# Kernel optimization log

Measured on AMD Instinct MI355X. Metric: run time of the kernel, lower is better.

## Reference

```python
import jax, jax.numpy as jnp
import numpy as np

B, P, V, M = 4, 4, 4096, 2048
BIG = 1e10  # masking constant for invalid points in min-reductions


def setup_inputs() -> dict:
    key = jax.random.key(0)
    k1, k2, k3, k4, k5 = jax.random.split(key, 5)
    vertices = jax.random.normal(k1, (B, V, 3), jnp.float32)
    # 3x4 projection matrices; force the 3rd row so w = 0.05*z + 4 > 0 (no divide blowup)
    projmats = 0.5 * jax.random.normal(k2, (P, 3, 4), jnp.float32)
    projmats = projmats.at[:, 2, :].set(jnp.array([0.0, 0.0, 0.05, 4.0], jnp.float32))
    edgemaps = jax.random.normal(k3, (B, P, M, 2), jnp.float32)
    boundary_mask = jax.random.bernoulli(k4, 0.3, (B, P, V))
    edgemaps_len = jax.random.randint(k5, (B, P), M // 2, M + 1, jnp.int32)
    return {"vertices": vertices, "projmats": projmats, "edgemaps": edgemaps,
            "boundary_mask": boundary_mask, "edgemaps_len": edgemaps_len}


def reference(vertices, projmats, edgemaps, boundary_mask, edgemaps_len):
    # --- project vertices into all views (homogeneous + perspective divide) ---
    ones = jnp.ones(vertices.shape[:2] + (1,), vertices.dtype)
    vh = jnp.concatenate([vertices, ones], axis=-1)              # (B,V,4)
    proj = jnp.einsum('pij,bvj->bpvi', projmats, vh)             # (B,P,V,3)
    pts = proj[..., :2] / proj[..., 2:3]                         # (B,P,V,2)

    # --- masked pairwise squared distances (GEMM-form, no (.,.,2) broadcast) ---
    x2 = jnp.sum(pts * pts, axis=-1)                             # (B,P,V)
    y2 = jnp.sum(edgemaps * edgemaps, axis=-1)                   # (B,P,M)
    xy = jnp.einsum('bpvc,bpmc->bpvm', pts, edgemaps)            # (B,P,V,M)
    d2 = jnp.maximum(x2[..., :, None] + y2[..., None, :] - 2.0 * xy, 0.0)

    xmask = boundary_mask.astype(d2.dtype)                       # (B,P,V)
    ymask = (jnp.arange(M)[None, None, :] < edgemaps_len[..., None]).astype(d2.dtype)

    # min over valid targets / valid boundary points
    cham_x = jnp.min(jnp.where(ymask[:, :, None, :] > 0, d2, BIG), axis=-1)  # (B,P,V)
    cham_y = jnp.min(jnp.where(xmask[:, :, :, None] > 0, d2, BIG), axis=-2)  # (B,P,M)

    x_len = jnp.maximum(jnp.sum(xmask, axis=-1), 1.0)            # (B,P)
    y_len = jnp.maximum(jnp.sum(ymask, axis=-1), 1.0)            # (B,P)
    loss_p = jnp.sum(xmask * cham_x, -1) / x_len + jnp.sum(ymask * cham_y, -1) / y_len
    return jnp.mean(loss_p, axis=-1)                             # (B,) per-mesh chamfer loss
```

## Files before the change

kernel.cpp:

```cpp
#include <hip/hip_runtime.h>
#include <stdint.h>

namespace {
constexpr int B = 4, P = 4, V = 4096, M = 2048;
constexpr int BP = B * P;
constexpr float BIGF = 1e10f;
constexpr int TPB   = 256;
constexpr int OTILE = 128;
constexpr int XT = V / OTILE;
constexpr int YT = M / OTILE;
constexpr int ROLES = XT + YT;
constexpr int NBLK = BP * ROLES;
constexpr int UN = 8;
constexpr int KPB = 4;
constexpr int VPB = V / KPB;
constexpr int MPB = M / KPB;
}


__global__ __launch_bounds__(256) void prep_kernel(
    const float* __restrict__ vertices,
    const float* __restrict__ projmats,
    const uint8_t* __restrict__ maskraw,
    const float* __restrict__ edgemaps,
    int* __restrict__ nvalid,
    float* __restrict__ sx,
    float* __restrict__ sy,
    int* __restrict__ done,
    float4* __restrict__ pnk,
    float4* __restrict__ epk)
{
    const int bp = blockIdx.x / KPB;
    const int k  = blockIdx.x % KPB;
    const int b = bp / P, p = bp % P;
    const int tid = threadIdx.x;
    const int lane = tid & 63;
    const int wave = tid >> 6;

    __shared__ int s_res[4];
    __shared__ int s_cnt;
    __shared__ int s_prew[4];
    if (tid < 4) { s_res[tid] = 0; s_prew[tid] = 0; }
    if (tid == 0) s_cnt = 0;
    __syncthreads();

    uint32_t loc[4] = {0u, 0u, 0u, 0u};
    const int NB = 16384;
    for (int i = tid * 16; i < NB; i += 256 * 16) {
        const uint32_t* w = (const uint32_t*)(maskraw + i);
        const uint32_t orw = w[0] | w[1] | w[2] | w[3];
        loc[0] |= orw & 0x000000FFu;
        loc[1] |= orw & 0x0000FF00u;
        loc[2] |= orw & 0x00FF0000u;
        loc[3] |= orw & 0xFF000000u;
    }
    #pragma unroll
    for (int j = 0; j < 4; ++j)
        if (loc[j]) atomicOr(&s_res[j], 1);
    __syncthreads();
    int layout;
    if (!s_res[1] && !s_res[2] && !s_res[3]) layout = 1;
    else if (!s_res[0] && !s_res[1])         layout = 2;
    else                                      layout = 0;

    {
        const float2* eg = (const float2*)edgemaps + (size_t)bp * M;
        for (int m = k * MPB + tid; m < (k + 1) * MPB; m += 256) {
            const float2 e = eg[m];
            epk[(size_t)bp * M + m] =
                make_float4(e.x, e.y, fmaf(e.x, e.x, e.y * e.y), 0.f);
        }
    }

    const int pre_n = k * VPB;
    int cnt = 0;
    if (layout == 0) {
        const uint8_t* mk = maskraw + (size_t)bp * V;
        for (int i = tid; i < pre_n; i += 256) cnt += (mk[i] != 0);
    } else if (layout == 1) {
        const int* mk = (const int*)maskraw + (size_t)bp * V;
        for (int i = tid; i < pre_n; i += 256) cnt += (mk[i] != 0);
    } else {
        const float* mk = (const float*)maskraw + (size_t)bp * V;
        for (int i = tid; i < pre_n; i += 256) cnt += (mk[i] != 0.0f);
    }
    #pragma unroll
    for (int off = 32; off > 0; off >>= 1) cnt += __shfl_down(cnt, off, 64);
    if (lane == 0) s_prew[wave] = cnt;
    __syncthreads();
    const int pre_total = s_prew[0] + s_prew[1] + s_prew[2] + s_prew[3];

    float mm[12];
    #pragma unroll
    for (int j = 0; j < 12; ++j) mm[j] = projmats[p * 12 + j];

    for (int v = k * VPB + tid; v < (k + 1) * VPB; v += 256) {
        const int mi = bp * V + v;
        bool msk;
        if (layout == 0)      msk = maskraw[mi] != 0;
        else if (layout == 1) msk = ((const int*)maskraw)[mi] != 0;
        else                  msk = ((const float*)maskraw)[mi] != 0.0f;

        const unsigned long long ball = __ballot(msk);
        const int bcnt = __popcll(ball);
        int base = 0;
        if (lane == 0 && bcnt) base = atomicAdd(&s_cnt, bcnt);
        base = __shfl(base, 0, 64);
        if (msk) {
            const float x = vertices[(b * V + v) * 3 + 0];
            const float y = vertices[(b * V + v) * 3 + 1];
            const float z = vertices[(b * V + v) * 3 + 2];
            const float u  = mm[0]*x + mm[1]*y + mm[2]*z  + mm[3];
            const float vv = mm[4]*x + mm[5]*y + mm[6]*z  + mm[7];
            const float w  = mm[8]*x + mm[9]*y + mm[10]*z + mm[11];
            const int off = __popcll(ball & ((1ull << lane) - 1ull));
            const float rw = 1.0f / w;
            const float px = u * rw, py = vv * rw;
            pnk[(size_t)bp * V + pre_total + base + off] =
                make_float4(px, py, fmaf(px, px, py * py), 0.f);
        }
    }
    __syncthreads();
    if (tid == 0) {
        if (k == KPB - 1) nvalid[bp] = pre_total + s_cnt;
        if (k == 0) { sx[bp] = 0.0f; sy[bp] = 0.0f; }
        if (blockIdx.x == 0) *done = 0;
    }
}

__global__ __launch_bounds__(TPB) void chamfer_kernel(
    const int* __restrict__ elen,
    int* __restrict__ nvalid,
    float* __restrict__ sx,
    float* __restrict__ sy,
    int* __restrict__ done,
    const float4* __restrict__ pnk,
    const float4* __restrict__ epk,
    float* __restrict__ out)
{
    const int bp   = blockIdx.x;
    const int role = blockIdx.y;
    const int tid  = threadIdx.x;
    const int wave = tid >> 6;
    const int lane = tid & 63;
    const int len  = elen[bp];
    const int nv   = nvalid[bp];

    __shared__ float  smin[4][OTILE];
    __shared__ int    s_last;

    const float4* outer; const float4* inner;
    int lim, L, obase;
    float* acc;
    const bool isX = (role < XT);
    if (isX) {
        obase = role * OTILE;
        outer = pnk + (size_t)bp * V;  lim = nv;
        inner = epk + (size_t)bp * M;  L = len;
        acc = &sx[bp];
    } else {
        obase = (role - XT) * OTILE;
        outer = epk + (size_t)bp * M;  lim = len;
        inner = pnk + (size_t)bp * V;  L = nv;
        acc = &sy[bp];
    }
    const bool active = (obase < lim);

    float pn0 = 0.f, pn1 = 0.f;
    if (active) {
        const float4 p0 = outer[obase + lane];
        const float4 p1 = outer[obase + 64 + lane];
        const float a0 = -2.0f * p0.x, b0 = -2.0f * p0.y;  pn0 = p0.z;
        const float a1 = -2.0f * p1.x, b1 = -2.0f * p1.y;  pn1 = p1.z;

        const int q = (L + 3) >> 2;
        const int is = wave * q;
        const int ie = min(is + q, L);

        float mn0 = BIGF, mn1 = BIGF;
        int j = is;
        for (; j + UN <= ie; j += UN) {
            float4 t[UN];
            #pragma unroll
            for (int u = 0; u < UN; ++u) t[u] = inner[j + u];
            #pragma unroll
            for (int u = 0; u < UN; ++u) {
                mn0 = fminf(mn0, fmaf(t[u].x, a0, fmaf(t[u].y, b0, t[u].z)));
                mn1 = fminf(mn1, fmaf(t[u].x, a1, fmaf(t[u].y, b1, t[u].z)));
            }
        }
        for (; j < ie; ++j) {
            const float4 t = inner[j];
            mn0 = fminf(mn0, fmaf(t.x, a0, fmaf(t.y, b0, t.z)));
            mn1 = fminf(mn1, fmaf(t.x, a1, fmaf(t.y, b1, t.z)));
        }
        smin[wave][lane]      = mn0;
        smin[wave][64 + lane] = mn1;
    }
    __syncthreads();
    if (active && wave == 0) {
        const float m0 = fminf(fminf(smin[0][lane],      smin[1][lane]),
                               fminf(smin[2][lane],      smin[3][lane]));
        const float m1 = fminf(fminf(smin[0][64 + lane], smin[1][64 + lane]),
                               fminf(smin[2][64 + lane], smin[3][64 + lane]));
        float val = 0.0f;
        if (obase + lane < lim)      val += fmaxf(m0 + pn0, 0.0f);
        if (obase + 64 + lane < lim) val += fmaxf(m1 + pn1, 0.0f);
        #pragma unroll
        for (int off = 32; off > 0; off >>= 1)
            val += __shfl_down(val, off, 64);
        if (lane == 0) atomicAdd(acc, val);
    }

    __syncthreads();
    if (tid == 0) {
        __threadfence();
        const int old = atomicAdd(done, 1);
        s_last = (old == NBLK - 1) ? 1 : 0;
    }
    __syncthreads();
    if (s_last) {
        __threadfence();
        if (tid < B) {
            float o = 0.0f;
            #pragma unroll
            for (int p = 0; p < P; ++p) {
                const int j = tid * P + p;
                o += sx[j] / fmaxf((float)nvalid[j], 1.0f)
                   + sy[j] / fmaxf((float)elen[j], 1.0f);
            }
            out[tid] = o * (1.0f / P);
        }
    }
}

extern "C" void kernel_launch(void* const* d_in, const int* in_sizes, int n_in,
                              void* d_out, int out_size, void* d_ws, size_t ws_size,
                              hipStream_t stream)
{
    const float*   vertices = (const float*)d_in[0];
    const float*   projmats = (const float*)d_in[1];
    const float*   edgemaps = (const float*)d_in[2];
    const uint8_t* maskraw  = (const uint8_t*)d_in[3];
    const int*     elen     = (const int*)d_in[4];
    float* out = (float*)d_out;

    char* ws = (char*)d_ws;
    int*    nvalid = (int*)(ws + 0);
    float*  sx     = (float*)(ws + 64);
    float*  sy     = (float*)(ws + 128);
    int*    done   = (int*)(ws + 192);
    float4* pnk    = (float4*)(ws + 256);
    float4* epk    = pnk + (size_t)BP * V;

    prep_kernel<<<BP * KPB, 256, 0, stream>>>(vertices, projmats, maskraw,
                                              edgemaps, nvalid, sx, sy, done,
                                              pnk, epk);
    chamfer_kernel<<<dim3(BP, ROLES), TPB, 0, stream>>>(elen, nvalid, sx, sy,
                                                        done, pnk, epk, out);
}
```

Measured before the change: 102.6 us.

## Register-block outer points per wave and pad inner lists with sentinels

Restructures the chamfer inner loop. Each wave now holds 16 outer points broadcast into registers via readlane, and each lane walks the inner points, so every loaded inner point is reused across 16 outer points. Before, each lane held two outer points and streamed the whole inner range. Inner arrays are padded to multiples of 128 with BIG-norm sentinels, which removes tail handling and masking. Pre-scaled transposed copies (-2x, -2y, norm) are written in prep. A two-stage shared-memory min reduction replaces the per-wave combine, and prep splits across more blocks per view. The cost is extra workspace traffic, larger register pressure from 16 accumulators, and padded iterations.

```diff
diff --git a/kernel.cpp b/kernel.cpp
--- a/kernel.cpp
+++ b/kernel.cpp
@@ -6,13 +6,13 @@
 constexpr int BP = B * P;
 constexpr float BIGF = 1e10f;
 constexpr int TPB   = 256;
-constexpr int OTILE = 128;
+constexpr int OTILE = 64;
+constexpr int OPW   = 16;
 constexpr int XT = V / OTILE;
 constexpr int YT = M / OTILE;
 constexpr int ROLES = XT + YT;
 constexpr int NBLK = BP * ROLES;
-constexpr int UN = 8;
-constexpr int KPB = 4;
+constexpr int KPB = 8;
 constexpr int VPB = V / KPB;
 constexpr int MPB = M / KPB;
 }
@@ -23,12 +23,15 @@
     const float* __restrict__ projmats,
     const uint8_t* __restrict__ maskraw,
     const float* __restrict__ edgemaps,
+    const int* __restrict__ elen,
     int* __restrict__ nvalid,
     float* __restrict__ sx,
     float* __restrict__ sy,
     int* __restrict__ done,
     float4* __restrict__ pnk,
-    float4* __restrict__ epk)
+    float4* __restrict__ epk,
+    float4* __restrict__ pnT,
+    float4* __restrict__ epT)
 {
     const int bp = blockIdx.x / KPB;
     const int k  = blockIdx.x % KPB;
@@ -63,12 +66,17 @@
     else if (!s_res[0] && !s_res[1])         layout = 2;
     else                                      layout = 0;
 
+    const int len = elen[bp];
+
     {
         const float2* eg = (const float2*)edgemaps + (size_t)bp * M;
         for (int m = k * MPB + tid; m < (k + 1) * MPB; m += 256) {
             const float2 e = eg[m];
+            const float n = fmaf(e.x, e.x, e.y * e.y);
             epk[(size_t)bp * M + m] =
-                make_float4(e.x, e.y, fmaf(e.x, e.x, e.y * e.y), 0.f);
+                make_float4(e.x, e.y, (m < len) ? n : BIGF, 0.f);
+            epT[(size_t)bp * M + m] =
+                make_float4(-2.0f * e.x, -2.0f * e.y, n, 0.f);
         }
     }
 
@@ -116,13 +124,21 @@
             const int off = __popcll(ball & ((1ull << lane) - 1ull));
             const float rw = 1.0f / w;
             const float px = u * rw, py = vv * rw;
-            pnk[(size_t)bp * V + pre_total + base + off] =
-                make_float4(px, py, fmaf(px, px, py * py), 0.f);
-        }
-    }
-    __syncthreads();
+            const float n  = fmaf(px, px, py * py);
+            const size_t dst = (size_t)bp * V + pre_total + base + off;
+            pnk[dst] = make_float4(px, py, n, 0.f);
+            pnT[dst] = make_float4(-2.0f * px, -2.0f * py, n, 0.f);
+        }
+    }
+    __syncthreads();
+    if (k == KPB - 1) {
+        const int nvv  = pre_total + s_cnt;
+        const int npad = (nvv + 127) & ~127;
+        for (int i = nvv + tid; i < npad; i += 256)
+            pnk[(size_t)bp * V + i] = make_float4(0.f, 0.f, BIGF, 0.f);
+        if (tid == 0) nvalid[bp] = nvv;
+    }
     if (tid == 0) {
-        if (k == KPB - 1) nvalid[bp] = pre_total + s_cnt;
         if (k == 0) { sx[bp] = 0.0f; sy[bp] = 0.0f; }
         if (blockIdx.x == 0) *done = 0;
     }
@@ -136,6 +152,8 @@
     int* __restrict__ done,
     const float4* __restrict__ pnk,
     const float4* __restrict__ epk,
+    const float4* __restrict__ pnT,
+    const float4* __restrict__ epT,
     float* __restrict__ out)
 {
     const int bp   = blockIdx.x;
@@ -146,66 +164,81 @@
     const int len  = elen[bp];
     const int nv   = nvalid[bp];
 
-    __shared__ float  smin[4][OTILE];
-    __shared__ int    s_last;
-
-    const float4* outer; const float4* inner;
+    __shared__ float sred[OTILE][65];
+    __shared__ float spart[OTILE][5];
+    __shared__ int   s_last;
+
+    const float4* outerT; const float4* inner;
     int lim, L, obase;
     float* acc;
     const bool isX = (role < XT);
     if (isX) {
         obase = role * OTILE;
-        outer = pnk + (size_t)bp * V;  lim = nv;
-        inner = epk + (size_t)bp * M;  L = len;
+        outerT = pnT + (size_t)bp * V;  lim = nv;
+        inner  = epk + (size_t)bp * M;  L = len;
         acc = &sx[bp];
     } else {
         obase = (role - XT) * OTILE;
-        outer = epk + (size_t)bp * M;  lim = len;
-        inner = pnk + (size_t)bp * V;  L = nv;
+        outerT = epT + (size_t)bp * M;  lim = len;
+        inner  = pnk + (size_t)bp * V;  L = nv;
         acc = &sy[bp];
     }
-    const bool active = (obase < lim);
-
-    float pn0 = 0.f, pn1 = 0.f;
+    const bool active = (obase < lim) && (L > 0);
+
     if (active) {
-        const float4 p0 = outer[obase + lane];
-        const float4 p1 = outer[obase + 64 + lane];
-        const float a0 = -2.0f * p0.x, b0 = -2.0f * p0.y;  pn0 = p0.z;
-        const float a1 = -2.0f * p1.x, b1 = -2.0f * p1.y;  pn1 = p1.z;
-
-        const int q = (L + 3) >> 2;
-        const int is = wave * q;
-        const int ie = min(is + q, L);
-
-        float mn0 = BIGF, mn1 = BIGF;
-        int j = is;
-        for (; j + UN <= ie; j += UN) {
-            float4 t[UN];
+        const float4 op = outerT[obase + wave * OPW + (lane & (OPW - 1))];
+        float sa[OPW], sb[OPW];
+        #pragma unroll
+        for (int o = 0; o < OPW; ++o) {
+            sa[o] = __uint_as_float(
+                __builtin_amdgcn_readlane(__float_as_uint(op.x), o));
+            sb[o] = __uint_as_float(
+                __builtin_amdgcn_readlane(__float_as_uint(op.y), o));
+        }
+
+        float mn[OPW];
+        #pragma unroll
+        for (int o = 0; o < OPW; ++o) mn[o] = BIGF;
+
+        const int Lpad = (L + 127) & ~127;
+        float4 t0 = inner[lane];
+        float4 t1 = inner[64 + lane];
+        for (int c = 128; c < Lpad; c += 128) {
+            const float4 n0 = inner[c + lane];
+            const float4 n1 = inner[c + 64 + lane];
             #pragma unroll
-            for (int u = 0; u < UN; ++u) t[u] = inner[j + u];
+            for (int o = 0; o < OPW; ++o)
+                mn[o] = fminf(mn[o], fmaf(t0.x, sa[o], fmaf(t0.y, sb[o], t0.z)));
             #pragma unroll
-            for (int u = 0; u < UN; ++u) {
-                mn0 = fminf(mn0, fmaf(t[u].x, a0, fmaf(t[u].y, b0, t[u].z)));
-                mn1 = fminf(mn1, fmaf(t[u].x, a1, fmaf(t[u].y, b1, t[u].z)));
-            }
-        }
-        for (; j < ie; ++j) {
-            const float4 t = inner[j];
-            mn0 = fminf(mn0, fmaf(t.x, a0, fmaf(t.y, b0, t.z)));
-            mn1 = fminf(mn1, fmaf(t.x, a1, fmaf(t.y, b1, t.z)));
-        }
-        smin[wave][lane]      = mn0;
-        smin[wave][64 + lane] = mn1;
+            for (int o = 0; o < OPW; ++o)
+                mn[o] = fminf(mn[o], fmaf(t1.x, sa[o], fmaf(t1.y, sb[o], t1.z)));
+            t0 = n0; t1 = n1;
+        }
+        #pragma unroll
+        for (int o = 0; o < OPW; ++o)
+            mn[o] = fminf(mn[o], fmaf(t0.x, sa[o], fmaf(t0.y, sb[o], t0.z)));
+        #pragma unroll
+        for (int o = 0; o < OPW; ++o)
+            mn[o] = fminf(mn[o], fmaf(t1.x, sa[o], fmaf(t1.y, sb[o], t1.z)));
+
+        #pragma unroll
+        for (int o = 0; o < OPW; ++o)
+            sred[wave * OPW + o][lane] = mn[o];
+    }
+    __syncthreads();
+    if (active) {
+        const int og = tid >> 2, seg = tid & 3;
+        float m = sred[og][seg * 16];
+        #pragma unroll
+        for (int i = 1; i < 16; ++i) m = fminf(m, sred[og][seg * 16 + i]);
+        spart[og][seg] = m;
     }
     __syncthreads();
     if (active && wave == 0) {
-        const float m0 = fminf(fminf(smin[0][lane],      smin[1][lane]),
-                               fminf(smin[2][lane],      smin[3][lane]));
-        const float m1 = fminf(fminf(smin[0][64 + lane], smin[1][64 + lane]),
-                               fminf(smin[2][64 + lane], smin[3][64 + lane]));
-        float val = 0.0f;
-        if (obase + lane < lim)      val += fmaxf(m0 + pn0, 0.0f);
-        if (obase + 64 + lane < lim) val += fmaxf(m1 + pn1, 0.0f);
+        const float m = fminf(fminf(spart[lane][0], spart[lane][1]),
+                              fminf(spart[lane][2], spart[lane][3]));
+        const float npv = outerT[obase + lane].z;
+        float val = (obase + lane < lim) ? fmaxf(m + npv, 0.0f) : 0.0f;
         #pragma unroll
         for (int off = 32; off > 0; off >>= 1)
             val += __shfl_down(val, off, 64);
@@ -252,10 +285,13 @@
     int*    done   = (int*)(ws + 192);
     float4* pnk    = (float4*)(ws + 256);
     float4* epk    = pnk + (size_t)BP * V;
+    float4* pnT    = epk + (size_t)BP * M;
+    float4* epT    = pnT + (size_t)BP * V;
 
     prep_kernel<<<BP * KPB, 256, 0, stream>>>(vertices, projmats, maskraw,
-                                              edgemaps, nvalid, sx, sy, done,
-                                              pnk, epk);
+                                              edgemaps, elen, nvalid, sx, sy,
+                                              done, pnk, epk, pnT, epT);
     chamfer_kernel<<<dim3(BP, ROLES), TPB, 0, stream>>>(elen, nvalid, sx, sy,
-                                                        done, pnk, epk, out);
-}
+                                                        done, pnk, epk, pnT,
+                                                        epT, out);
+}
```

Result: no change. 101.9 us (-0.7%).
